# Optimization experiments

Measured on AMD Instinct MI355X. Metric: run time of the kernel, lower is better.

The kernel has to match this reference:

```python
import jax, jax.numpy as jnp
import numpy as np

B, S, E, H, D = 2, 2048, 768, 12, 64  # batch, seq, emb_dim, num_heads, encoder_emb_dim
EPS = 1e-5


def setup_inputs() -> dict:
    key = jax.random.key(0)
    ks = jax.random.split(key, 6)
    # kaiming-uniform-ish bound for fan_in=E
    bound = float(np.sqrt(6.0 / E))
    u = lambda k, shp: jax.random.uniform(k, shp, jnp.float32, -bound, bound)
    return {
        "x": jax.random.normal(ks[0], (B, S, E), jnp.float32),
        "ln_w": jnp.ones((E,), jnp.float32),
        "ln_b": jnp.zeros((E,), jnp.float32),
        "wq": u(ks[1], (E, H * D)),
        "bq": jnp.zeros((H * D,), jnp.float32),
        "wk": u(ks[2], (E, H * D)),
        "bk": jnp.zeros((H * D,), jnp.float32),
        "wv": u(ks[3], (E, H * D)),
        "bv": jnp.zeros((H * D,), jnp.float32),
        "wo": u(ks[4], (H * D, E)),
        "bo": jnp.zeros((E,), jnp.float32),
    }


def reference(x, ln_w, ln_b, wq, bq, wk, bk, wv, bv, wo, bo):
    b, s, _ = x.shape
    # LayerNorm (biased variance, eps=1e-5), as torch.nn.LayerNorm
    mu = x.mean(-1, keepdims=True)
    var = ((x - mu) ** 2).mean(-1, keepdims=True)
    xn = (x - mu) * jax.lax.rsqrt(var + EPS) * ln_w + ln_b

    q = (xn @ wq + bq).reshape(b, s, H, D)
    k = (xn @ wk + bk).reshape(b, s, H, D)
    v = (xn @ wv + bv).reshape(b, s, H, D)

    scale = 1.0 / np.sqrt(D).astype(np.float32)
    scores = jnp.einsum("bihd,bjhd->bhij", q, k) * scale  # [B,H,S,S]

    # masking=True, self_attending=True: mask STRICTLY lower triangle with -inf
    # (i.e. each position attends only to itself and FUTURE positions)
    mask = jnp.tril(jnp.ones((s, s), dtype=bool), k=-1)
    scores = jnp.where(mask, -jnp.inf, scores)

    a = jax.nn.softmax(scores, axis=-1)
    h = jnp.einsum("bhij,bjhd->bihd", a, v).reshape(b, s, H * D)
    return h @ wo + bo
```

## Files before the change

### kernel.cpp

```cpp
#include <hip/hip_runtime.h>

typedef __bf16 bf16_t;
typedef __bf16 bf16x8 __attribute__((ext_vector_type(8)));
typedef __bf16 bf16x4 __attribute__((ext_vector_type(4)));
typedef short  s16x4  __attribute__((ext_vector_type(4)));
typedef float  f32x4  __attribute__((ext_vector_type(4)));
typedef unsigned int u32;

#define BB 2
#define SS 2048
#define EE 768
#define HH 12
#define DD 64
#define NROW (BB*SS)

#define GLDS16(gp, lp) __builtin_amdgcn_global_load_lds( \
    (const __attribute__((address_space(1))) u32*)(gp),   \
    (__attribute__((address_space(3))) u32*)(lp), 16, 0, 0)

#if __has_builtin(__builtin_amdgcn_mfma_f32_16x16x16bf16_1k)
#define MFMA16_BUILTIN 1
static __device__ __forceinline__ f32x4 mfma_16x16x16_bf16(bf16x4 a, bf16x4 b, f32x4 c) {
  return __builtin_amdgcn_mfma_f32_16x16x16bf16_1k(
      __builtin_bit_cast(s16x4, a), __builtin_bit_cast(s16x4, b), c, 0, 0, 0);
}
#else
#define MFMA16_BUILTIN 0
static __device__ __forceinline__ f32x4 mfma_16x16x16_bf16(bf16x4 a, bf16x4 b, f32x4 c) {
  asm volatile("v_mfma_f32_16x16x16_bf16 %0, %1, %2, %0" : "+v"(c) : "v"(a), "v"(b));
  return c;
}
#endif

__global__ __launch_bounds__(256) void pack_w_kernel(
    const float* __restrict__ wq, const float* __restrict__ wk,
    const float* __restrict__ wv, const float* __restrict__ wo,
    bf16_t* __restrict__ wt)
{
  __shared__ float tile[64][65];
  const float* src = (blockIdx.z==0)?wq:(blockIdx.z==1)?wk:(blockIdx.z==2)?wv:wo;
  const int k0 = blockIdx.x*64, n0 = blockIdx.y*64;
  const int t = threadIdx.x;
  #pragma unroll
  for (int it=0; it<16; ++it) {
    int idx = it*256+t, r = idx>>6, c = idx&63;
    tile[r][c] = src[(size_t)(k0+r)*EE + n0 + c];
  }
  __syncthreads();
  bf16_t* dst = wt + (size_t)blockIdx.z*EE*EE;
  #pragma unroll
  for (int it=0; it<16; ++it) {
    int idx = it*256+t, r = idx>>6, c = idx&63;
    dst[(size_t)(n0+r)*EE + k0 + c] = (bf16_t)tile[c][r];
  }
}

__global__ __launch_bounds__(256) void ln_kernel(
    const float* __restrict__ x, const float* __restrict__ w,
    const float* __restrict__ bvec, bf16_t* __restrict__ xn)
{
  const int row = blockIdx.x, t = threadIdx.x;
  const float* xr = x + (size_t)row*EE;
  float v0 = xr[t], v1 = xr[t+256], v2 = xr[t+512];
  float s  = v0+v1+v2;
  float ss = v0*v0 + v1*v1 + v2*v2;
  #pragma unroll
  for (int m=1; m<64; m<<=1) { s += __shfl_xor(s,m); ss += __shfl_xor(ss,m); }
  __shared__ float red[2][4];
  const int wid = t>>6, lane = t&63;
  if (lane==0) { red[0][wid]=s; red[1][wid]=ss; }
  __syncthreads();
  s  = red[0][0]+red[0][1]+red[0][2]+red[0][3];
  ss = red[1][0]+red[1][1]+red[1][2]+red[1][3];
  const float mu   = s*(1.0f/EE);
  const float rstd = rsqrtf(ss*(1.0f/EE) - mu*mu + 1e-5f);
  bf16_t* xo = xn + (size_t)row*EE;
  xo[t      ] = (bf16_t)((v0-mu)*rstd*w[t      ] + bvec[t      ]);
  xo[t + 256] = (bf16_t)((v1-mu)*rstd*w[t + 256] + bvec[t + 256]);
  xo[t + 512] = (bf16_t)((v2-mu)*rstd*w[t + 512] + bvec[t + 512]);
}

__global__ __launch_bounds__(256) void gemm_qkv_kernel(
    const bf16_t* __restrict__ xn, const bf16_t* __restrict__ wt,
    const float* __restrict__ bq, const float* __restrict__ bk, const float* __restrict__ bv,
    bf16_t* __restrict__ qb, bf16_t* __restrict__ kb, bf16_t* __restrict__ vb)
{
  __shared__ __align__(16) bf16_t As[2][128][32];
  __shared__ __align__(16) bf16_t Bs[2][96][32];
  const int bm = blockIdx.x, by = blockIdx.y;
  const int mat = by >> 3, nb = by & 7;
  const bf16_t* W = wt + (size_t)mat*EE*EE + (size_t)nb*96*EE;
  const float* bias = (mat==0)?bq:(mat==1)?bk:bv;
  bf16_t* outp = (mat==0)?qb:(mat==1)?kb:vb;
  const int t = threadIdx.x, lane = t&63, wid = t>>6;
  const int wr = wid>>1, wc = wid&1;
  const int lrow = lane&15, lk = lane>>4;
  const bf16_t* Ag = xn + (size_t)bm*128*EE;

  const int srow = t>>2, sp = t&3;
  const int sg = sp ^ ((srow>>1)&3);
  const int pcs = (lrow>>1)&3;

  auto stage = [&](int buf, int k0) {
    const bf16_t* asrc = Ag + (size_t)srow*EE + k0 + sg*8;
    const bf16_t* bsrc = W  + (size_t)srow*EE + k0 + sg*8;
    GLDS16(asrc,                 &As[buf][0][0] + t*8);
    GLDS16(asrc + (size_t)64*EE, &As[buf][0][0] + 2048 + t*8);
    GLDS16(bsrc,                 &Bs[buf][0][0] + t*8);
    if (t < 128)
      GLDS16(bsrc + (size_t)64*EE, &Bs[buf][0][0] + 2048 + t*8);
  };

  f32x4 acc[4][3];
  #pragma unroll
  for (int i=0;i<4;++i)
    #pragma unroll
    for (int j=0;j<3;++j) acc[i][j] = (f32x4){0.f,0.f,0.f,0.f};

  stage(0, 0);
  __syncthreads();
  int cur = 0;
  for (int k0=0; k0<EE; k0+=32) {
    if (k0+32 < EE) stage(cur^1, k0+32);
    bf16x8 af[4], bfv[3];
    #pragma unroll
    for (int mi=0;mi<4;++mi) af[mi]  = *(const bf16x8*)&As[cur][wr*64+mi*16+lrow][(lk^pcs)*8];
    #pragma unroll
    for (int ni=0;ni<3;++ni) bfv[ni] = *(const bf16x8*)&Bs[cur][wc*48+ni*16+lrow][(lk^pcs)*8];
    #pragma unroll
    for (int mi=0;mi<4;++mi)
      #pragma unroll
      for (int ni=0;ni<3;++ni)
        acc[mi][ni] = __builtin_amdgcn_mfma_f32_16x16x32_bf16(af[mi], bfv[ni], acc[mi][ni], 0,0,0);
    __syncthreads();
    cur ^= 1;
  }
  const int m_base = bm*128 + wr*64;
  const int n_base = nb*96 + wc*48;
  #pragma unroll
  for (int ni=0;ni<3;++ni) {
    const int col = n_base + ni*16 + lrow;
    const float bias_v = bias[col];
    #pragma unroll
    for (int mi=0;mi<4;++mi) {
      #pragma unroll
      for (int r=0;r<4;++r) {
        int row = m_base + mi*16 + 4*lk + r;
        outp[(size_t)row*EE + col] = (bf16_t)(acc[mi][ni][r] + bias_v);
      }
    }
  }
}

__global__ __launch_bounds__(256) void vtrans_kernel(
    const bf16_t* __restrict__ v, bf16_t* __restrict__ vt)
{
  __shared__ __align__(16) bf16_t tile[64][72];
  const int j0 = blockIdx.x*64, bh = blockIdx.y;
  const int b = bh/HH, h = bh%HH;
  const int t = threadIdx.x;
  #pragma unroll
  for (int it=0; it<2; ++it) {
    int idx = it*256+t, r = idx>>3, c8 = (idx&7)*8;
    *(bf16x8*)&tile[r][c8] = *(const bf16x8*)(v + (size_t)(b*SS + j0 + r)*EE + h*DD + c8);
  }
  __syncthreads();
  #pragma unroll
  for (int it=0; it<2; ++it) {
    int idx = it*256+t, d = idx>>3, c8 = (idx&7)*8;
    bf16x8 val;
    #pragma unroll
    for (int i=0;i<8;++i) val[i] = tile[c8+i][d];
    *(bf16x8*)(vt + ((size_t)bh*DD + d)*SS + j0 + c8) = val;
  }
}

__global__ __launch_bounds__(256, 3) void attn_kernel(
    const bf16_t* __restrict__ qb, const bf16_t* __restrict__ kb,
    const bf16_t* __restrict__ vt, bf16_t* __restrict__ hb)
{
  __shared__ __align__(16) bf16_t Ks[2][64][64];
  __shared__ __align__(16) bf16_t Vts[2][64][64];
  __shared__ __align__(16) float  Osum[64][68];
  __shared__ float Lsum[4][64];

  const int bid = blockIdx.x;
  const int rnd = bid >> 8, g8 = bid & 255;
  const int item = (rnd == 1) ? (511 - g8) : (rnd*256 + g8);
  const int qt = item / 24, bh = item % 24;

  const int i0 = qt*64, b = bh/HH, h = bh%HH;
  const int t = threadIdx.x, lane = t&63, w = t>>6;
  const int lrow = lane&15, lk = lane>>4;

  const int sr = t>>3, sp = t&7;
  const int sgc = sp ^ (sr&7);
  const bf16_t* kbase  = kb + (size_t)b*SS*EE + h*DD;
  const bf16_t* vtbase = vt + (size_t)bh*DD*SS;

  bf16x8 qf[4][2];
  #pragma unroll
  for (int g=0; g<4; ++g) {
    const bf16_t* qrow = qb + (size_t)(b*SS + i0 + g*16 + lrow)*EE + h*DD;
    qf[g][0] = *(const bf16x8*)(qrow + lk*8);
    qf[g][1] = *(const bf16x8*)(qrow + 32 + lk*8);
  }

  f32x4 acc[4][4];
  #pragma unroll
  for (int g=0; g<4; ++g)
    #pragma unroll
    for (int i=0;i<4;++i) acc[g][i] = (f32x4){0.f,0.f,0.f,0.f};
  float lsum[4] = {0.f,0.f,0.f,0.f};
  const int kkey = lrow&7;

  auto stage = [&](int buf, int jt) {
    const int j0v = jt*64;
    const bf16_t* ksrc = kbase  + (size_t)(j0v + sr)*EE + sgc*8;
    const bf16_t* vsrc = vtbase + (size_t)sr*SS + j0v + sgc*8;
    GLDS16(ksrc,                 &Ks[buf][0][0]  + t*8);
    GLDS16(ksrc + (size_t)32*EE, &Ks[buf][0][0]  + 2048 + t*8);
    GLDS16(vsrc,                 &Vts[buf][0][0] + t*8);
    GLDS16(vsrc + (size_t)32*SS, &Vts[buf][0][0] + 2048 + t*8);
  };

#define ATTN_TILE(CUR, MASKED) do {                                          \
    const bf16_t* krow = &Ks[CUR][w*16 + lrow][0];                           \
    bf16x8 kf0 = *(const bf16x8*)(krow + ((lk^kkey)<<3));                    \
    bf16x8 kf1 = *(const bf16x8*)(krow + (((lk+4)^kkey)<<3));                \
    bf16x4 pb[4];                                                            \
    _Pragma("unroll")                                                        \
    for (int g=0; g<4; ++g) {                                                \
      f32x4 a = (f32x4){0.f,0.f,0.f,0.f};                                    \
      a = __builtin_amdgcn_mfma_f32_16x16x32_bf16(kf0, qf[g][0], a, 0,0,0);  \
      a = __builtin_amdgcn_mfma_f32_16x16x32_bf16(kf1, qf[g][1], a, 0,0,0);  \
      _Pragma("unroll")                                                      \
      for (int r=0;r<4;++r) {                                                \
        float ee = a[r]*0.180336878f - 34.6246784f;                          \
        if (MASKED && (w*16 + 4*lk + r) < (g*16 + lrow)) ee = -1e30f;        \
        float p = exp2f(ee);                                                 \
        lsum[g] += p;                                                        \
        pb[g][r] = (bf16_t)p;                                                \
      }                                                                      \
    }                                                                        \
    _Pragma("unroll")                                                        \
    for (int sd=0;sd<4;++sd) {                                               \
      const bf16_t* vrow = &Vts[CUR][sd*16+lrow][0];                         \
      bf16x4 vf = *(const bf16x4*)(vrow + (((2*w+(lk>>1))^kkey)<<3) + ((lk&1)<<2)); \
      _Pragma("unroll")                                                      \
      for (int g=0; g<4; ++g)                                                \
        acc[g][sd] = mfma_16x16x16_bf16(vf, pb[g], acc[g][sd]);              \
    }                                                                        \
  } while(0)

  const int ntiles = SS/64 - qt;
  stage(0, qt);
  __syncthreads();
  if (ntiles > 1) stage(1, qt+1);
  ATTN_TILE(0, true);
#if !MFMA16_BUILTIN
  asm volatile("s_nop 7\n\ts_nop 7");
#endif
  __syncthreads();

  int cur = 1;
  for (int it2=1; it2<ntiles; ++it2) {
    if (it2+1 < ntiles) stage(cur^1, qt+it2+1);
    ATTN_TILE(cur, false);
#if !MFMA16_BUILTIN
    asm volatile("s_nop 7\n\ts_nop 7");
#endif
    __syncthreads();
    cur ^= 1;
  }
#undef ATTN_TILE

  #pragma unroll
  for (int g=0; g<4; ++g) {
    lsum[g] += __shfl_xor(lsum[g], 16);
    lsum[g] += __shfl_xor(lsum[g], 32);
  }
  if (lane < 16) {
    #pragma unroll
    for (int g=0; g<4; ++g) Lsum[w][g*16 + lane] = lsum[g];
  }

  __syncthreads();
  if (w == 0) {
    #pragma unroll
    for (int g=0; g<4; ++g)
      #pragma unroll
      for (int sd=0; sd<4; ++sd)
        *(f32x4*)&Osum[g*16+lrow][sd*16 + 4*lk] = acc[g][sd];
  }
  __syncthreads();
  if (w == 1) {
    #pragma unroll
    for (int g=0; g<4; ++g)
      #pragma unroll
      for (int sd=0; sd<4; ++sd) {
        f32x4 v = *(f32x4*)&Osum[g*16+lrow][sd*16 + 4*lk];
        *(f32x4*)&Osum[g*16+lrow][sd*16 + 4*lk] = v + acc[g][sd];
      }
  }
  __syncthreads();
  if (w == 2) {
    #pragma unroll
    for (int g=0; g<4; ++g)
      #pragma unroll
      for (int sd=0; sd<4; ++sd) {
        f32x4 v = *(f32x4*)&Osum[g*16+lrow][sd*16 + 4*lk];
        *(f32x4*)&Osum[g*16+lrow][sd*16 + 4*lk] = v + acc[g][sd];
      }
  }
  __syncthreads();
  if (w == 3) {
    #pragma unroll
    for (int g=0; g<4; ++g)
      #pragma unroll
      for (int sd=0; sd<4; ++sd) {
        f32x4 v = *(f32x4*)&Osum[g*16+lrow][sd*16 + 4*lk];
        *(f32x4*)&Osum[g*16+lrow][sd*16 + 4*lk] = v + acc[g][sd];
      }
  }
  __syncthreads();

  const int q = t>>2, dq = t&3;
  const float ltot = Lsum[0][q] + Lsum[1][q] + Lsum[2][q] + Lsum[3][q];
  const float inv = 1.0f / ltot;
  bf16_t* orow = hb + (size_t)(b*SS + i0 + q)*EE + h*DD + dq*16;
  bf16x8 o0, o1;
  #pragma unroll
  for (int c=0;c<2;++c) {
    f32x4 v0 = *(const f32x4*)&Osum[q][dq*16 + c*8];
    f32x4 v1 = *(const f32x4*)&Osum[q][dq*16 + c*8 + 4];
    #pragma unroll
    for (int i=0;i<4;++i) {
      if (c==0) { o0[i] = (bf16_t)(v0[i]*inv); o0[i+4] = (bf16_t)(v1[i]*inv); }
      else      { o1[i] = (bf16_t)(v0[i]*inv); o1[i+4] = (bf16_t)(v1[i]*inv); }
    }
  }
  *(bf16x8*)orow = o0;
  *(bf16x8*)(orow+8) = o1;
}

__global__ __launch_bounds__(256) void gemm_out_kernel(
    const bf16_t* __restrict__ hbuf, const bf16_t* __restrict__ wto,
    const float* __restrict__ bo, float* __restrict__ out)
{
  __shared__ __align__(16) bf16_t As[2][64][32];
  __shared__ __align__(16) bf16_t Bs[2][96][32];
  const int bm = blockIdx.x, nb = blockIdx.y;
  const bf16_t* W = wto + (size_t)nb*96*EE;
  const int t = threadIdx.x, lane = t&63, wid = t>>6;
  const int wr = wid>>1, wc = wid&1;
  const int lrow = lane&15, lk = lane>>4;
  const bf16_t* Ag = hbuf + (size_t)bm*64*EE;

  const int srow = t>>2, sp = t&3;
  const int sg = sp ^ ((srow>>1)&3);
  const int pcs = (lrow>>1)&3;

  auto stage = [&](int buf, int k0) {
    const bf16_t* asrc = Ag + (size_t)srow*EE + k0 + sg*8;
    const bf16_t* bsrc = W  + (size_t)srow*EE + k0 + sg*8;
    GLDS16(asrc, &As[buf][0][0] + t*8);
    GLDS16(bsrc, &Bs[buf][0][0] + t*8);
    if (t < 128)
      GLDS16(bsrc + (size_t)64*EE, &Bs[buf][0][0] + 2048 + t*8);
  };

  f32x4 acc[2][3];
  #pragma unroll
  for (int i=0;i<2;++i)
    #pragma unroll
    for (int j=0;j<3;++j) acc[i][j] = (f32x4){0.f,0.f,0.f,0.f};

  stage(0, 0);
  __syncthreads();
  int cur = 0;
  for (int k0=0; k0<EE; k0+=32) {
    if (k0+32 < EE) stage(cur^1, k0+32);
    bf16x8 af[2], bfv[3];
    #pragma unroll
    for (int mi=0;mi<2;++mi) af[mi]  = *(const bf16x8*)&As[cur][wr*32+mi*16+lrow][(lk^pcs)*8];
    #pragma unroll
    for (int ni=0;ni<3;++ni) bfv[ni] = *(const bf16x8*)&Bs[cur][wc*48+ni*16+lrow][(lk^pcs)*8];
    #pragma unroll
    for (int mi=0;mi<2;++mi)
      #pragma unroll
      for (int ni=0;ni<3;++ni)
        acc[mi][ni] = __builtin_amdgcn_mfma_f32_16x16x32_bf16(af[mi], bfv[ni], acc[mi][ni], 0,0,0);
    __syncthreads();
    cur ^= 1;
  }
  const int m_base = bm*64 + wr*32;
  const int n_base = nb*96 + wc*48;
  #pragma unroll
  for (int ni=0;ni<3;++ni) {
    const int col = n_base + ni*16 + lrow;
    const float bias_v = bo[col];
    #pragma unroll
    for (int mi=0;mi<2;++mi) {
      #pragma unroll
      for (int r=0;r<4;++r) {
        int row = m_base + mi*16 + 4*lk + r;
        out[(size_t)row*EE + col] = acc[mi][ni][r] + bias_v;
      }
    }
  }
}

extern "C" void kernel_launch(void* const* d_in, const int* in_sizes, int n_in,
                              void* d_out, int out_size, void* d_ws, size_t ws_size,
                              hipStream_t stream) {
  const float* x    = (const float*)d_in[0];
  const float* ln_w = (const float*)d_in[1];
  const float* ln_b = (const float*)d_in[2];
  const float* wq   = (const float*)d_in[3];
  const float* bq   = (const float*)d_in[4];
  const float* wk   = (const float*)d_in[5];
  const float* bk   = (const float*)d_in[6];
  const float* wv   = (const float*)d_in[7];
  const float* bv   = (const float*)d_in[8];
  const float* wo   = (const float*)d_in[9];
  const float* bo   = (const float*)d_in[10];
  float* out = (float*)d_out;

  char* ws = (char*)d_ws;
  bf16_t* wt  = (bf16_t*)(ws);
  bf16_t* xn  = (bf16_t*)(ws + 4718592);
  bf16_t* qb  = (bf16_t*)(ws + 11010048);
  bf16_t* kb  = (bf16_t*)(ws + 17301504);
  bf16_t* vb  = (bf16_t*)(ws + 23592960);
  bf16_t* vtb = (bf16_t*)(ws + 29884416);
  bf16_t* hb  = (bf16_t*)(ws + 36175872);

  pack_w_kernel  <<<dim3(12,12,4), 256, 0, stream>>>(wq, wk, wv, wo, wt);
  ln_kernel      <<<dim3(NROW),    256, 0, stream>>>(x, ln_w, ln_b, xn);
  gemm_qkv_kernel<<<dim3(32,24),   256, 0, stream>>>(xn, wt, bq, bk, bv, qb, kb, vb);
  vtrans_kernel  <<<dim3(32,24),   256, 0, stream>>>(vb, vtb);
  attn_kernel    <<<dim3(768),     256, 0, stream>>>(qb, kb, vtb, hb);
  gemm_out_kernel<<<dim3(64,8),    256, 0, stream>>>(hb, wt + (size_t)3*EE*EE, bo, out);
}
```

Baseline: 89.75 us.

## Triple-buffer K/V tiles in attention with one vmcnt-gated barrier per tile

The attention kernel now keeps three LDS buffers for K and V^T tiles instead of two and prefetches two tiles ahead. Each iteration uses a single partial s_waitcnt vmcnt plus a barrier in place of the two __syncthreads, so the next loads stay in flight while the current tile is computed. The Osum reduction scratch is aliased onto the K buffers to offset part of the added LDS. The hard-coded vmcnt(4) assumes stage() issues exactly four global loads per thread, and the larger LDS footprint may lower occupancy below the launch-bounds target of three blocks per CU.

```diff
diff --git a/kernel.cpp b/kernel.cpp
--- a/kernel.cpp
+++ b/kernel.cpp
@@ -17,6 +17,13 @@
 #define GLDS16(gp, lp) __builtin_amdgcn_global_load_lds( \
     (const __attribute__((address_space(1))) u32*)(gp),   \
     (__attribute__((address_space(3))) u32*)(lp), 16, 0, 0)
+
+static __device__ __forceinline__ void pipe_wait(bool more_in_flight) {
+  if (more_in_flight) asm volatile("s_waitcnt vmcnt(4)" ::: "memory");
+  else                asm volatile("s_waitcnt vmcnt(0)" ::: "memory");
+  __builtin_amdgcn_s_barrier();
+  asm volatile("" ::: "memory");
+}
 
 #if __has_builtin(__builtin_amdgcn_mfma_f32_16x16x16bf16_1k)
 #define MFMA16_BUILTIN 1
@@ -179,9 +186,8 @@
     const bf16_t* __restrict__ qb, const bf16_t* __restrict__ kb,
     const bf16_t* __restrict__ vt, bf16_t* __restrict__ hb)
 {
-  __shared__ __align__(16) bf16_t Ks[2][64][64];
-  __shared__ __align__(16) bf16_t Vts[2][64][64];
-  __shared__ __align__(16) float  Osum[64][68];
+  __shared__ __align__(16) bf16_t Ks[3][64][64];
+  __shared__ __align__(16) bf16_t Vts[3][64][64];
   __shared__ float Lsum[4][64];
 
   const int bid = blockIdx.x;
@@ -255,23 +261,27 @@
 
   const int ntiles = SS/64 - qt;
   stage(0, qt);
-  __syncthreads();
   if (ntiles > 1) stage(1, qt+1);
+
+  pipe_wait(ntiles > 1);
+  if (2 < ntiles) stage(2, qt+2);
   ATTN_TILE(0, true);
 #if !MFMA16_BUILTIN
   asm volatile("s_nop 7\n\ts_nop 7");
 #endif
-  __syncthreads();
-
-  int cur = 1;
+
+  int bufi = 1;
   for (int it2=1; it2<ntiles; ++it2) {
-    if (it2+1 < ntiles) stage(cur^1, qt+it2+1);
-    ATTN_TILE(cur, false);
+    pipe_wait(it2+1 < ntiles);
+    if (it2+2 < ntiles) {
+      int nb2 = (bufi >= 1) ? bufi-1 : 2;
+      stage(nb2, qt+it2+2);
+    }
+    ATTN_TILE(bufi, false);
 #if !MFMA16_BUILTIN
     asm volatile("s_nop 7\n\ts_nop 7");
 #endif
-    __syncthreads();
-    cur ^= 1;
+    bufi = (bufi==2) ? 0 : bufi+1;
   }
 #undef ATTN_TILE
 
@@ -280,18 +290,20 @@
     lsum[g] += __shfl_xor(lsum[g], 16);
     lsum[g] += __shfl_xor(lsum[g], 32);
   }
+  __syncthreads();
   if (lane < 16) {
     #pragma unroll
     for (int g=0; g<4; ++g) Lsum[w][g*16 + lane] = lsum[g];
   }
 
+  float* OS = (float*)&Ks[0][0][0];
   __syncthreads();
   if (w == 0) {
     #pragma unroll
     for (int g=0; g<4; ++g)
       #pragma unroll
       for (int sd=0; sd<4; ++sd)
-        *(f32x4*)&Osum[g*16+lrow][sd*16 + 4*lk] = acc[g][sd];
+        *(f32x4*)&OS[(g*16+lrow)*68 + sd*16 + 4*lk] = acc[g][sd];
   }
   __syncthreads();
   if (w == 1) {
@@ -299,8 +311,8 @@
     for (int g=0; g<4; ++g)
       #pragma unroll
       for (int sd=0; sd<4; ++sd) {
-        f32x4 v = *(f32x4*)&Osum[g*16+lrow][sd*16 + 4*lk];
-        *(f32x4*)&Osum[g*16+lrow][sd*16 + 4*lk] = v + acc[g][sd];
+        f32x4 v = *(f32x4*)&OS[(g*16+lrow)*68 + sd*16 + 4*lk];
+        *(f32x4*)&OS[(g*16+lrow)*68 + sd*16 + 4*lk] = v + acc[g][sd];
       }
   }
   __syncthreads();
@@ -309,8 +321,8 @@
     for (int g=0; g<4; ++g)
       #pragma unroll
       for (int sd=0; sd<4; ++sd) {
-        f32x4 v = *(f32x4*)&Osum[g*16+lrow][sd*16 + 4*lk];
-        *(f32x4*)&Osum[g*16+lrow][sd*16 + 4*lk] = v + acc[g][sd];
+        f32x4 v = *(f32x4*)&OS[(g*16+lrow)*68 + sd*16 + 4*lk];
+        *(f32x4*)&OS[(g*16+lrow)*68 + sd*16 + 4*lk] = v + acc[g][sd];
       }
   }
   __syncthreads();
@@ -319,8 +331,8 @@
     for (int g=0; g<4; ++g)
       #pragma unroll
       for (int sd=0; sd<4; ++sd) {
-        f32x4 v = *(f32x4*)&Osum[g*16+lrow][sd*16 + 4*lk];
-        *(f32x4*)&Osum[g*16+lrow][sd*16 + 4*lk] = v + acc[g][sd];
+        f32x4 v = *(f32x4*)&OS[(g*16+lrow)*68 + sd*16 + 4*lk];
+        *(f32x4*)&OS[(g*16+lrow)*68 + sd*16 + 4*lk] = v + acc[g][sd];
       }
   }
   __syncthreads();
@@ -332,8 +344,8 @@
   bf16x8 o0, o1;
   #pragma unroll
   for (int c=0;c<2;++c) {
-    f32x4 v0 = *(const f32x4*)&Osum[q][dq*16 + c*8];
-    f32x4 v1 = *(const f32x4*)&Osum[q][dq*16 + c*8 + 4];
+    f32x4 v0 = *(const f32x4*)&OS[q*68 + dq*16 + c*8];
+    f32x4 v1 = *(const f32x4*)&OS[q*68 + dq*16 + c*8 + 4];
     #pragma unroll
     for (int i=0;i<4;++i) {
       if (c==0) { o0[i] = (bf16_t)(v0[i]*inv); o0[i+4] = (bf16_t)(v1[i]*inv); }
```

Measured after the change: 90.85 us. Within noise of the previous version (+1.2%).

## Give each wave private K/V LDS slices and drop per-tile block barriers

Applied to the files above, without the earlier changes.

Re-partitions the shared K and V^T tiles so each wave stages only the 16 keys it consumes into its own LDS region, using a new swizzle and a V layout packed for the MFMA operand reads. Because no wave reads data loaded by another, the per-tile __syncthreads is replaced by s_waitcnt vmcnt on the wave's own async global-to-LDS loads. This removes block-wide barrier stalls between waves in the attention loop. It relies on vmcnt correctly covering the global_load_lds writes to LDS before they are read. The V reads may also now hit LDS bank conflicts.

```diff
diff --git a/kernel.cpp b/kernel.cpp
--- a/kernel.cpp
+++ b/kernel.cpp
@@ -179,8 +179,8 @@
     const bf16_t* __restrict__ qb, const bf16_t* __restrict__ kb,
     const bf16_t* __restrict__ vt, bf16_t* __restrict__ hb)
 {
-  __shared__ __align__(16) bf16_t Ks[2][64][64];
-  __shared__ __align__(16) bf16_t Vts[2][64][64];
+  __shared__ __align__(16) bf16_t Kw[4][2][1024];
+  __shared__ __align__(16) bf16_t Vw[4][2][1024];
   __shared__ __align__(16) float  Osum[64][68];
   __shared__ float Lsum[4][64];
 
@@ -193,8 +193,6 @@
   const int t = threadIdx.x, lane = t&63, w = t>>6;
   const int lrow = lane&15, lk = lane>>4;
 
-  const int sr = t>>3, sp = t&7;
-  const int sgc = sp ^ (sr&7);
   const bf16_t* kbase  = kb + (size_t)b*SS*EE + h*DD;
   const bf16_t* vtbase = vt + (size_t)bh*DD*SS;
 
@@ -214,18 +212,19 @@
   float lsum[4] = {0.f,0.f,0.f,0.f};
   const int kkey = lrow&7;
 
+  const int ksh = ((lane&7) ^ (lane>>3)) << 3;
   auto stage = [&](int buf, int jt) {
     const int j0v = jt*64;
-    const bf16_t* ksrc = kbase  + (size_t)(j0v + sr)*EE + sgc*8;
-    const bf16_t* vsrc = vtbase + (size_t)sr*SS + j0v + sgc*8;
-    GLDS16(ksrc,                 &Ks[buf][0][0]  + t*8);
-    GLDS16(ksrc + (size_t)32*EE, &Ks[buf][0][0]  + 2048 + t*8);
-    GLDS16(vsrc,                 &Vts[buf][0][0] + t*8);
-    GLDS16(vsrc + (size_t)32*SS, &Vts[buf][0][0] + 2048 + t*8);
+    const bf16_t* k0 = kbase + (size_t)(j0v + w*16 + (lane>>3))*EE + ksh;
+    GLDS16(k0,                &Kw[w][buf][lane*8]);
+    GLDS16(k0 + (size_t)8*EE, &Kw[w][buf][512 + lane*8]);
+    const bf16_t* v0 = vtbase + (size_t)(lane>>1)*SS + j0v + w*16 + ((lane&1)<<3);
+    GLDS16(v0,                 &Vw[w][buf][lane*8]);
+    GLDS16(v0 + (size_t)32*SS, &Vw[w][buf][512 + lane*8]);
   };
 
 #define ATTN_TILE(CUR, MASKED) do {                                          \
-    const bf16_t* krow = &Ks[CUR][w*16 + lrow][0];                           \
+    const bf16_t* krow = &Kw[w][CUR][lrow*64];                               \
     bf16x8 kf0 = *(const bf16x8*)(krow + ((lk^kkey)<<3));                    \
     bf16x8 kf1 = *(const bf16x8*)(krow + (((lk+4)^kkey)<<3));                \
     bf16x4 pb[4];                                                            \
@@ -245,8 +244,7 @@
     }                                                                        \
     _Pragma("unroll")                                                        \
     for (int sd=0;sd<4;++sd) {                                               \
-      const bf16_t* vrow = &Vts[CUR][sd*16+lrow][0];                         \
-      bf16x4 vf = *(const bf16x4*)(vrow + (((2*w+(lk>>1))^kkey)<<3) + ((lk&1)<<2)); \
+      bf16x4 vf = *(const bf16x4*)&Vw[w][CUR][(sd*16+lrow)*16 + lk*4];       \
       _Pragma("unroll")                                                      \
       for (int g=0; g<4; ++g)                                                \
         acc[g][sd] = mfma_16x16x16_bf16(vf, pb[g], acc[g][sd]);              \
@@ -255,23 +253,17 @@
 
   const int ntiles = SS/64 - qt;
   stage(0, qt);
-  __syncthreads();
-  if (ntiles > 1) stage(1, qt+1);
-  ATTN_TILE(0, true);
-#if !MFMA16_BUILTIN
-  asm volatile("s_nop 7\n\ts_nop 7");
-#endif
-  __syncthreads();
-
-  int cur = 1;
-  for (int it2=1; it2<ntiles; ++it2) {
-    if (it2+1 < ntiles) stage(cur^1, qt+it2+1);
-    ATTN_TILE(cur, false);
+  for (int t2=0; t2<ntiles; ++t2) {
+    if (t2+1 < ntiles) {
+      stage((t2+1)&1, qt+t2+1);
+      asm volatile("s_waitcnt vmcnt(4)" ::: "memory");
+    } else {
+      asm volatile("s_waitcnt vmcnt(0)" ::: "memory");
+    }
+    if (t2 == 0) { ATTN_TILE((t2&1), true); } else { ATTN_TILE((t2&1), false); }
 #if !MFMA16_BUILTIN
     asm volatile("s_nop 7\n\ts_nop 7");
 #endif
-    __syncthreads();
-    cur ^= 1;
   }
 #undef ATTN_TILE
 
```

Result: no change. 90.22 us (+0.5%).
